# Kernel tuning notes

Hardware: AMD Instinct MI355X
Metric: run time of the kernel (lower is better)

The kernel has to match this reference:

```python
import jax, jax.numpy as jnp
import numpy as np

EPS = 1e-8  # torch cosine_similarity eps


def setup_inputs() -> dict:
    key = jax.random.key(0)
    kx, kw = jax.random.split(key)
    B, D, C, K = 512, 512, 5994, 3
    x = jax.random.normal(kx, (B, D), dtype=jnp.float32)
    # xavier_normal over (D, C, K): std = sqrt(2 / (fan_in + fan_out))
    std = float(np.sqrt(2.0 / (D + C * K)))
    W = jax.random.normal(kw, (D, C, K), dtype=jnp.float32) * std
    return {"x": x, "W": W}


def reference(x, W):
    # cosine similarity along feature dim, without materializing [B, D, C, K]
    x_norm = jnp.maximum(jnp.linalg.norm(x, axis=1, keepdims=True), EPS)   # [B, 1]
    w_norm = jnp.maximum(jnp.linalg.norm(W, axis=0, keepdims=True), EPS)   # [1, C, K]
    xn = x / x_norm                                                        # [B, D]
    Wn = W / w_norm                                                        # [D, C, K]
    costh = jnp.einsum('bd,dck->bck', xn, Wn)                              # [B, C, K]
    return costh
```

## Files before the change

### kernel.cpp

```cpp
#include <hip/hip_runtime.h>
#include <hip/hip_bf16.h>
#include <stdint.h>


#define D_DIM 512
#define BM 128
#define BN 128
#define NG (D_DIM / 8)
#define NSTEPS (D_DIM / 32)
#define TILE_BYTES (NG * BM * 16)

typedef __bf16 bf16x8 __attribute__((ext_vector_type(8)));
typedef float f32x4 __attribute__((ext_vector_type(4)));

__device__ __forceinline__ unsigned short f2bf(float f) {
  union { float f; unsigned int u; } v; v.f = f;
  unsigned int u = v.u;
  u += 0x7fffu + ((u >> 16) & 1u);
  return (unsigned short)(u >> 16);
}

__device__ __forceinline__ void load_lds16(const void* g, void* l) {
  __builtin_amdgcn_global_load_lds(
      (__attribute__((address_space(1))) void*)(g),
      (__attribute__((address_space(3))) void*)(l), 16, 0, 0);
}

__global__ void xnorm_kernel(const float* __restrict__ x, unsigned short* __restrict__ An) {
  const int m = blockIdx.x;
  const int t = threadIdx.x;
  const float* xr = x + (size_t)m * D_DIM + t * 8;
  float4 a = *(const float4*)(xr);
  float4 b = *(const float4*)(xr + 4);
  float s = a.x * a.x + a.y * a.y + a.z * a.z + a.w * a.w +
            b.x * b.x + b.y * b.y + b.z * b.z + b.w * b.w;
#pragma unroll
  for (int off = 32; off; off >>= 1) s += __shfl_xor(s, off, 64);
  const float inv = 1.f / fmaxf(sqrtf(s), 1e-8f);
  ushort4 o0, o1;
  o0.x = f2bf(a.x * inv); o0.y = f2bf(a.y * inv); o0.z = f2bf(a.z * inv); o0.w = f2bf(a.w * inv);
  o1.x = f2bf(b.x * inv); o1.y = f2bf(b.y * inv); o1.z = f2bf(b.z * inv); o1.w = f2bf(b.w * inv);
  const int mtile = m >> 7, r = m & 127;
  unsigned short* dst = An + (size_t)mtile * (TILE_BYTES / 2) + (size_t)t * (BM * 8) + r * 8;
  *(ushort4*)dst = o0;
  *(ushort4*)(dst + 4) = o1;
}

__global__ void wtrans2_kernel(const float* __restrict__ W, unsigned short* __restrict__ Wt,
                               float* __restrict__ partial, int CK, int NT128) {
  __shared__ unsigned short tile[64][128];
  __shared__ float red[256 * 4];
  const int t = threadIdx.x;
  const int ntile = blockIdx.x, gb = blockIdx.y;
  const int n0 = ntile * BN;
  const int cq = t & 31;
  const int dr = t >> 5;
  const int d_base = gb * 64;
  float ss0 = 0.f, ss1 = 0.f, ss2 = 0.f, ss3 = 0.f;

  if (n0 + BN <= CK) {
#pragma unroll
    for (int i = 0; i < 8; ++i) {
      const int dl = dr + i * 8;
      float4 v = *(const float4*)(W + (size_t)(d_base + dl) * CK + n0 + cq * 4);
      ss0 += v.x * v.x; ss1 += v.y * v.y; ss2 += v.z * v.z; ss3 += v.w * v.w;
      ushort4 o; o.x = f2bf(v.x); o.y = f2bf(v.y); o.z = f2bf(v.z); o.w = f2bf(v.w);
      *(ushort4*)&tile[dl][cq * 4] = o;
    }
  } else {
#pragma unroll
    for (int i = 0; i < 8; ++i) {
      const int dl = dr + i * 8;
      float v[4];
#pragma unroll
      for (int e = 0; e < 4; ++e) {
        int n = n0 + cq * 4 + e;
        v[e] = W[(size_t)(d_base + dl) * CK + (n < CK ? n : CK - 1)];
      }
      ss0 += v[0] * v[0]; ss1 += v[1] * v[1]; ss2 += v[2] * v[2]; ss3 += v[3] * v[3];
      ushort4 o; o.x = f2bf(v[0]); o.y = f2bf(v[1]); o.z = f2bf(v[2]); o.w = f2bf(v[3]);
      *(ushort4*)&tile[dl][cq * 4] = o;
    }
  }
  red[t * 4 + 0] = ss0; red[t * 4 + 1] = ss1; red[t * 4 + 2] = ss2; red[t * 4 + 3] = ss3;
  __syncthreads();

  if (t < 128) {
    float s = 0.f;
#pragma unroll
    for (int k = 0; k < 8; ++k) s += red[k * 128 + t];
    partial[(size_t)gb * NT128 + n0 + t] = s;
  }

  unsigned short* outBase = Wt + (size_t)ntile * (TILE_BYTES / 2);
#pragma unroll
  for (int i = 0; i < 4; ++i) {
    const int idx = t + 256 * i;
    const int g = idx >> 7, r = idx & 127;
    ushort4 o0, o1;
    o0.x = tile[g * 8 + 0][r]; o0.y = tile[g * 8 + 1][r];
    o0.z = tile[g * 8 + 2][r]; o0.w = tile[g * 8 + 3][r];
    o1.x = tile[g * 8 + 4][r]; o1.y = tile[g * 8 + 5][r];
    o1.z = tile[g * 8 + 6][r]; o1.w = tile[g * 8 + 7][r];
    unsigned short* dst = outBase + (size_t)(gb * 8 + g) * (BM * 8) + r * 8;
    *(ushort4*)dst = o0;
    *(ushort4*)(dst + 4) = o1;
  }
}

__global__ __launch_bounds__(256, 2) void gemm_kernel(const unsigned short* __restrict__ An,
                                                      const unsigned short* __restrict__ Wt,
                                                      const float* __restrict__ partial,
                                                      float* __restrict__ out, int CK, int NT128) {
  __shared__ __attribute__((aligned(16))) unsigned char lds[16384];
  unsigned char* ldsA = lds;
  unsigned char* ldsB = lds + 8192;
  const int ntile = blockIdx.x, mtile = blockIdx.y;
  const int t = threadIdx.x;
  const int lane = t & 63, w = t >> 6;
  const int wm = w >> 1, wn = w & 1;
  const int lrow = lane & 15;
  const int g = lane >> 4;

  const unsigned char* srcA = (const unsigned char*)An + (size_t)mtile * TILE_BYTES;
  const unsigned char* srcB = (const unsigned char*)Wt + (size_t)ntile * TILE_BYTES;

  f32x4 acc[4][4] = {};

  for (int kt = 0; kt < NSTEPS; ++kt) {
    const size_t koff = (size_t)kt * 8192;
#pragma unroll
    for (int c = 0; c < 2; ++c) {
      const int off = w * 2048 + c * 1024;
      load_lds16(srcA + koff + off + lane * 16, ldsA + off);
      load_lds16(srcB + koff + off + lane * 16, ldsB + off);
    }
    __syncthreads();
    bf16x8 afrag[4], bfrag[4];
#pragma unroll
    for (int i = 0; i < 4; ++i) {
      afrag[i] = *(const bf16x8*)(ldsA + g * 2048 + (wm * 64 + i * 16 + lrow) * 16);
      bfrag[i] = *(const bf16x8*)(ldsB + g * 2048 + (wn * 64 + i * 16 + lrow) * 16);
    }
#pragma unroll
    for (int i = 0; i < 4; ++i)
#pragma unroll
      for (int j = 0; j < 4; ++j)
        acc[i][j] = __builtin_amdgcn_mfma_f32_16x16x32_bf16(afrag[i], bfrag[j], acc[i][j], 0, 0, 0);
    __syncthreads();
  }

  float* winv = (float*)lds;
  if (t < 128) {
    float s = 0.f;
#pragma unroll
    for (int k = 0; k < 8; ++k) s += partial[(size_t)k * NT128 + ntile * BN + t];
    winv[t] = 1.f / fmaxf(sqrtf(s), 1e-8f);
  }
  __syncthreads();

#pragma unroll
  for (int j = 0; j < 4; ++j) {
    const int cl = wn * 64 + j * 16 + lrow;
    const int col = ntile * BN + cl;
    if (col < CK) {
      const float wv = winv[cl];
#pragma unroll
      for (int i = 0; i < 4; ++i) {
#pragma unroll
        for (int jj = 0; jj < 4; ++jj) {
          const int row = mtile * BM + wm * 64 + i * 16 + g * 4 + jj;
          out[(size_t)row * CK + col] = acc[i][j][jj] * wv;
        }
      }
    }
  }
}

extern "C" void kernel_launch(void* const* d_in, const int* in_sizes, int n_in,
                              void* d_out, int out_size, void* d_ws, size_t ws_size,
                              hipStream_t stream) {
  const float* x = (const float*)d_in[0];
  const float* W = (const float*)d_in[1];
  float* out = (float*)d_out;
  const int Bn = in_sizes[0] / D_DIM;
  const int CK = in_sizes[1] / D_DIM;
  const int ntiles = (CK + BN - 1) / BN;
  const int mtiles = Bn / BM;
  const int NT128 = ntiles * BN;

  unsigned char* ws = (unsigned char*)d_ws;
  float* partial = (float*)ws;
  unsigned short* An = (unsigned short*)(ws + 655360);
  unsigned short* Wt = (unsigned short*)(ws + 655360 + (size_t)mtiles * TILE_BYTES);

  hipLaunchKernelGGL(xnorm_kernel, dim3(Bn), dim3(64), 0, stream, x, An);
  hipLaunchKernelGGL(wtrans2_kernel, dim3(ntiles, 8), dim3(256), 0, stream, W, Wt, partial, CK, NT128);
  hipLaunchKernelGGL(gemm_kernel, dim3(ntiles, mtiles), dim3(256), 0, stream, An, Wt, partial, out, CK, NT128);
}
```

Measured before the change: 42.89 us.

## Fuse prep kernels, double-buffer GEMM K-loop with BK=64, XCD-aware tile mapping

Merges the x normalisation and W transpose/convert kernels into one prep launch. The W transpose now goes through registers instead of an LDS tile. The GEMM switches to a 64-wide K step with double-buffered LDS (64KB) so the next tile's global-to-LDS loads overlap MFMA work. It also remaps linear block ids so neighbouring tiles land on the same XCD. The larger LDS footprint may cap the two-blocks-per-CU occupancy, and the single sync per iteration relies on async LDS loads completing by the barrier.

```diff
diff --git a/kernel.cpp b/kernel.cpp
--- a/kernel.cpp
+++ b/kernel.cpp
@@ -6,9 +6,9 @@
 #define D_DIM 512
 #define BM 128
 #define BN 128
-#define NG (D_DIM / 8)
-#define NSTEPS (D_DIM / 32)
-#define TILE_BYTES (NG * BM * 16)
+#define BK 64
+#define KITERS (D_DIM / BK)
+#define TILE_BYTES (64 * BM * 16)
 
 typedef __bf16 bf16x8 __attribute__((ext_vector_type(8)));
 typedef float f32x4 __attribute__((ext_vector_type(4)));
@@ -26,83 +26,77 @@
       (__attribute__((address_space(3))) void*)(l), 16, 0, 0);
 }
 
-__global__ void xnorm_kernel(const float* __restrict__ x, unsigned short* __restrict__ An) {
-  const int m = blockIdx.x;
+__global__ void prep_kernel(const float* __restrict__ x, const float* __restrict__ W,
+                            unsigned short* __restrict__ An, unsigned short* __restrict__ Wt,
+                            float* __restrict__ partial, int CK, int NT128, int nWtBlocks) {
+  const int b = blockIdx.x;
   const int t = threadIdx.x;
-  const float* xr = x + (size_t)m * D_DIM + t * 8;
-  float4 a = *(const float4*)(xr);
-  float4 b = *(const float4*)(xr + 4);
-  float s = a.x * a.x + a.y * a.y + a.z * a.z + a.w * a.w +
-            b.x * b.x + b.y * b.y + b.z * b.z + b.w * b.w;
-#pragma unroll
-  for (int off = 32; off; off >>= 1) s += __shfl_xor(s, off, 64);
-  const float inv = 1.f / fmaxf(sqrtf(s), 1e-8f);
-  ushort4 o0, o1;
-  o0.x = f2bf(a.x * inv); o0.y = f2bf(a.y * inv); o0.z = f2bf(a.z * inv); o0.w = f2bf(a.w * inv);
-  o1.x = f2bf(b.x * inv); o1.y = f2bf(b.y * inv); o1.z = f2bf(b.z * inv); o1.w = f2bf(b.w * inv);
-  const int mtile = m >> 7, r = m & 127;
-  unsigned short* dst = An + (size_t)mtile * (TILE_BYTES / 2) + (size_t)t * (BM * 8) + r * 8;
-  *(ushort4*)dst = o0;
-  *(ushort4*)(dst + 4) = o1;
-}
-
-__global__ void wtrans2_kernel(const float* __restrict__ W, unsigned short* __restrict__ Wt,
-                               float* __restrict__ partial, int CK, int NT128) {
-  __shared__ unsigned short tile[64][128];
-  __shared__ float red[256 * 4];
-  const int t = threadIdx.x;
-  const int ntile = blockIdx.x, gb = blockIdx.y;
-  const int n0 = ntile * BN;
-  const int cq = t & 31;
-  const int dr = t >> 5;
-  const int d_base = gb * 64;
-  float ss0 = 0.f, ss1 = 0.f, ss2 = 0.f, ss3 = 0.f;
-
-  if (n0 + BN <= CK) {
-#pragma unroll
-    for (int i = 0; i < 8; ++i) {
-      const int dl = dr + i * 8;
-      float4 v = *(const float4*)(W + (size_t)(d_base + dl) * CK + n0 + cq * 4);
-      ss0 += v.x * v.x; ss1 += v.y * v.y; ss2 += v.z * v.z; ss3 += v.w * v.w;
-      ushort4 o; o.x = f2bf(v.x); o.y = f2bf(v.y); o.z = f2bf(v.z); o.w = f2bf(v.w);
-      *(ushort4*)&tile[dl][cq * 4] = o;
+  if (b < nWtBlocks) {
+    __shared__ float red[8 * 128];
+    const int ntile = b >> 3, gb = b & 7;
+    const int cq = t & 31, dr = t >> 5;
+    const int n0 = ntile * BN;
+    const int nb = n0 + cq * 4;
+    const int g = gb * 8 + dr;
+    float ss0 = 0.f, ss1 = 0.f, ss2 = 0.f, ss3 = 0.f;
+    unsigned int gr[4][4];
+    if (n0 + BN <= CK) {
+#pragma unroll
+      for (int i = 0; i < 8; i += 2) {
+        float4 v0 = *(const float4*)(W + (size_t)(g * 8 + i) * CK + nb);
+        float4 v1 = *(const float4*)(W + (size_t)(g * 8 + i + 1) * CK + nb);
+        ss0 += v0.x * v0.x + v1.x * v1.x; ss1 += v0.y * v0.y + v1.y * v1.y;
+        ss2 += v0.z * v0.z + v1.z * v1.z; ss3 += v0.w * v0.w + v1.w * v1.w;
+        gr[0][i >> 1] = (unsigned int)f2bf(v0.x) | ((unsigned int)f2bf(v1.x) << 16);
+        gr[1][i >> 1] = (unsigned int)f2bf(v0.y) | ((unsigned int)f2bf(v1.y) << 16);
+        gr[2][i >> 1] = (unsigned int)f2bf(v0.z) | ((unsigned int)f2bf(v1.z) << 16);
+        gr[3][i >> 1] = (unsigned int)f2bf(v0.w) | ((unsigned int)f2bf(v1.w) << 16);
+      }
+    } else {
+      float acc_ss[4] = {0.f, 0.f, 0.f, 0.f};
+#pragma unroll
+      for (int i = 0; i < 8; i += 2) {
+#pragma unroll
+        for (int e = 0; e < 4; ++e) {
+          const int n = nb + e;
+          const float f0 = (n < CK) ? W[(size_t)(g * 8 + i) * CK + n] : 0.f;
+          const float f1 = (n < CK) ? W[(size_t)(g * 8 + i + 1) * CK + n] : 0.f;
+          acc_ss[e] += f0 * f0 + f1 * f1;
+          gr[e][i >> 1] = (unsigned int)f2bf(f0) | ((unsigned int)f2bf(f1) << 16);
+        }
+      }
+      ss0 = acc_ss[0]; ss1 = acc_ss[1]; ss2 = acc_ss[2]; ss3 = acc_ss[3];
+    }
+    unsigned short* dst = Wt + (size_t)ntile * (TILE_BYTES / 2) + (size_t)g * (BM * 8) + (size_t)cq * 32;
+#pragma unroll
+    for (int e = 0; e < 4; ++e) {
+      uint4 o; o.x = gr[e][0]; o.y = gr[e][1]; o.z = gr[e][2]; o.w = gr[e][3];
+      *(uint4*)(dst + e * 8) = o;
+    }
+    *(float4*)(&red[dr * 128 + cq * 4]) = make_float4(ss0, ss1, ss2, ss3);
+    __syncthreads();
+    if (t < 128) {
+      float s = 0.f;
+#pragma unroll
+      for (int k = 0; k < 8; ++k) s += red[k * 128 + t];
+      partial[(size_t)gb * NT128 + n0 + t] = s;
     }
   } else {
-#pragma unroll
-    for (int i = 0; i < 8; ++i) {
-      const int dl = dr + i * 8;
-      float v[4];
-#pragma unroll
-      for (int e = 0; e < 4; ++e) {
-        int n = n0 + cq * 4 + e;
-        v[e] = W[(size_t)(d_base + dl) * CK + (n < CK ? n : CK - 1)];
-      }
-      ss0 += v[0] * v[0]; ss1 += v[1] * v[1]; ss2 += v[2] * v[2]; ss3 += v[3] * v[3];
-      ushort4 o; o.x = f2bf(v[0]); o.y = f2bf(v[1]); o.z = f2bf(v[2]); o.w = f2bf(v[3]);
-      *(ushort4*)&tile[dl][cq * 4] = o;
-    }
-  }
-  red[t * 4 + 0] = ss0; red[t * 4 + 1] = ss1; red[t * 4 + 2] = ss2; red[t * 4 + 3] = ss3;
-  __syncthreads();
-
-  if (t < 128) {
-    float s = 0.f;
-#pragma unroll
-    for (int k = 0; k < 8; ++k) s += red[k * 128 + t];
-    partial[(size_t)gb * NT128 + n0 + t] = s;
-  }
-
-  unsigned short* outBase = Wt + (size_t)ntile * (TILE_BYTES / 2);
-#pragma unroll
-  for (int i = 0; i < 4; ++i) {
-    const int idx = t + 256 * i;
-    const int g = idx >> 7, r = idx & 127;
+    const int w = t >> 6, lane = t & 63;
+    const int m = (b - nWtBlocks) * 4 + w;
+    const float* xr = x + (size_t)m * D_DIM + lane * 8;
+    float4 a = *(const float4*)(xr);
+    float4 c = *(const float4*)(xr + 4);
+    float s = a.x * a.x + a.y * a.y + a.z * a.z + a.w * a.w +
+              c.x * c.x + c.y * c.y + c.z * c.z + c.w * c.w;
+#pragma unroll
+    for (int off = 32; off; off >>= 1) s += __shfl_xor(s, off, 64);
+    const float inv = 1.f / fmaxf(sqrtf(s), 1e-8f);
     ushort4 o0, o1;
-    o0.x = tile[g * 8 + 0][r]; o0.y = tile[g * 8 + 1][r];
-    o0.z = tile[g * 8 + 2][r]; o0.w = tile[g * 8 + 3][r];
-    o1.x = tile[g * 8 + 4][r]; o1.y = tile[g * 8 + 5][r];
-    o1.z = tile[g * 8 + 6][r]; o1.w = tile[g * 8 + 7][r];
-    unsigned short* dst = outBase + (size_t)(gb * 8 + g) * (BM * 8) + r * 8;
+    o0.x = f2bf(a.x * inv); o0.y = f2bf(a.y * inv); o0.z = f2bf(a.z * inv); o0.w = f2bf(a.w * inv);
+    o1.x = f2bf(c.x * inv); o1.y = f2bf(c.y * inv); o1.z = f2bf(c.z * inv); o1.w = f2bf(c.w * inv);
+    const int mtile = m >> 7, r = m & 127;
+    unsigned short* dst = An + (size_t)mtile * (TILE_BYTES / 2) + (size_t)lane * (BM * 8) + r * 8;
     *(ushort4*)dst = o0;
     *(ushort4*)(dst + 4) = o1;
   }
@@ -112,41 +106,67 @@
                                                       const unsigned short* __restrict__ Wt,
                                                       const float* __restrict__ partial,
                                                       float* __restrict__ out, int CK, int NT128) {
-  __shared__ __attribute__((aligned(16))) unsigned char lds[16384];
-  unsigned char* ldsA = lds;
-  unsigned char* ldsB = lds + 8192;
-  const int ntile = blockIdx.x, mtile = blockIdx.y;
+  __shared__ __attribute__((aligned(16))) unsigned char lds[65536];
+  const int total = gridDim.x;
+  const int q = total >> 3, rr = total & 7;
+  const int lin = blockIdx.x;
+  const int xcd = lin & 7, idx = lin >> 3;
+  const int wg = (xcd < rr) ? xcd * (q + 1) + idx : rr * (q + 1) + (xcd - rr) * q + idx;
+  const int ntile = wg >> 2, mtile = wg & 3;
+
   const int t = threadIdx.x;
   const int lane = t & 63, w = t >> 6;
   const int wm = w >> 1, wn = w & 1;
   const int lrow = lane & 15;
-  const int g = lane >> 4;
+  const int kg = lane >> 4;
 
   const unsigned char* srcA = (const unsigned char*)An + (size_t)mtile * TILE_BYTES;
   const unsigned char* srcB = (const unsigned char*)Wt + (size_t)ntile * TILE_BYTES;
+  const int n0 = ntile * BN;
 
   f32x4 acc[4][4] = {};
 
-  for (int kt = 0; kt < NSTEPS; ++kt) {
-    const size_t koff = (size_t)kt * 8192;
-#pragma unroll
-    for (int c = 0; c < 2; ++c) {
-      const int off = w * 2048 + c * 1024;
-      load_lds16(srcA + koff + off + lane * 16, ldsA + off);
-      load_lds16(srcB + koff + off + lane * 16, ldsB + off);
-    }
-    __syncthreads();
-    bf16x8 afrag[4], bfrag[4];
-#pragma unroll
-    for (int i = 0; i < 4; ++i) {
-      afrag[i] = *(const bf16x8*)(ldsA + g * 2048 + (wm * 64 + i * 16 + lrow) * 16);
-      bfrag[i] = *(const bf16x8*)(ldsB + g * 2048 + (wn * 64 + i * 16 + lrow) * 16);
-    }
+#define STAGE(kt, sel)                                                        \
+  {                                                                           \
+    const size_t koff = (size_t)(kt) * 16384;                                 \
+    unsigned char* bA = lds + (sel) * 32768;                                  \
+    unsigned char* bB = bA + 16384;                                           \
+    _Pragma("unroll")                                                         \
+    for (int c = 0; c < 4; ++c) {                                             \
+      const int off = w * 4096 + c * 1024;                                    \
+      load_lds16(srcA + koff + off + lane * 16, bA + off);                    \
+    }                                                                         \
+    _Pragma("unroll")                                                         \
+    for (int c = 0; c < 4; ++c) {                                             \
+      const int off = w * 4096 + c * 1024;                                    \
+      load_lds16(srcB + koff + off + lane * 16, bB + off);                    \
+    }                                                                         \
+  }
+
+  STAGE(0, 0);
+  __syncthreads();
+
+  for (int kt = 0; kt < KITERS; ++kt) {
+    const int cur = kt & 1;
+    if (kt + 1 < KITERS) STAGE(kt + 1, cur ^ 1);
+
+    const unsigned char* bA = lds + cur * 32768;
+    const unsigned char* bB = bA + 16384;
+    bf16x8 afrag[2][4], bfrag[2][4];
+#pragma unroll
+    for (int h = 0; h < 2; ++h)
+#pragma unroll
+      for (int i = 0; i < 4; ++i) {
+        afrag[h][i] = *(const bf16x8*)(bA + (kg + 4 * h) * 2048 + (wm * 64 + i * 16 + lrow) * 16);
+        bfrag[h][i] = *(const bf16x8*)(bB + (kg + 4 * h) * 2048 + (wn * 64 + i * 16 + lrow) * 16);
+      }
 #pragma unroll
     for (int i = 0; i < 4; ++i)
 #pragma unroll
-      for (int j = 0; j < 4; ++j)
-        acc[i][j] = __builtin_amdgcn_mfma_f32_16x16x32_bf16(afrag[i], bfrag[j], acc[i][j], 0, 0, 0);
+      for (int j = 0; j < 4; ++j) {
+        acc[i][j] = __builtin_amdgcn_mfma_f32_16x16x32_bf16(afrag[0][i], bfrag[0][j], acc[i][j], 0, 0, 0);
+        acc[i][j] = __builtin_amdgcn_mfma_f32_16x16x32_bf16(afrag[1][i], bfrag[1][j], acc[i][j], 0, 0, 0);
+      }
     __syncthreads();
   }
 
@@ -154,7 +174,7 @@
   if (t < 128) {
     float s = 0.f;
 #pragma unroll
-    for (int k = 0; k < 8; ++k) s += partial[(size_t)k * NT128 + ntile * BN + t];
+    for (int k = 0; k < 8; ++k) s += partial[(size_t)k * NT128 + n0 + t];
     winv[t] = 1.f / fmaxf(sqrtf(s), 1e-8f);
   }
   __syncthreads();
@@ -162,14 +182,14 @@
 #pragma unroll
   for (int j = 0; j < 4; ++j) {
     const int cl = wn * 64 + j * 16 + lrow;
-    const int col = ntile * BN + cl;
+    const int col = n0 + cl;
     if (col < CK) {
       const float wv = winv[cl];
 #pragma unroll
       for (int i = 0; i < 4; ++i) {
 #pragma unroll
         for (int jj = 0; jj < 4; ++jj) {
-          const int row = mtile * BM + wm * 64 + i * 16 + g * 4 + jj;
+          const int row = mtile * BM + wm * 64 + i * 16 + kg * 4 + jj;
           out[(size_t)row * CK + col] = acc[i][j][jj] * wv;
         }
       }
@@ -191,10 +211,13 @@
 
   unsigned char* ws = (unsigned char*)d_ws;
   float* partial = (float*)ws;
-  unsigned short* An = (unsigned short*)(ws + 655360);
-  unsigned short* Wt = (unsigned short*)(ws + 655360 + (size_t)mtiles * TILE_BYTES);
-
-  hipLaunchKernelGGL(xnorm_kernel, dim3(Bn), dim3(64), 0, stream, x, An);
-  hipLaunchKernelGGL(wtrans2_kernel, dim3(ntiles, 8), dim3(256), 0, stream, W, Wt, partial, CK, NT128);
-  hipLaunchKernelGGL(gemm_kernel, dim3(ntiles, mtiles), dim3(256), 0, stream, An, Wt, partial, out, CK, NT128);
-}
+  unsigned short* An = (unsigned short*)(ws + 8 * (size_t)NT128 * 4);
+  unsigned short* Wt = (unsigned short*)(ws + 8 * (size_t)NT128 * 4 + (size_t)mtiles * TILE_BYTES);
+
+  const int nWtBlocks = ntiles * 8;
+  const int nXBlocks = Bn / 4;
+  hipLaunchKernelGGL(prep_kernel, dim3(nWtBlocks + nXBlocks), dim3(256), 0, stream,
+                     x, W, An, Wt, partial, CK, NT128, nWtBlocks);
+  hipLaunchKernelGGL(gemm_kernel, dim3(ntiles * mtiles), dim3(256), 0, stream,
+                     An, Wt, partial, out, CK, NT128);
+}
```

Result: faster. 41.57 us (-3.1%).
